# Kernel tuning notes

Measured on AMD Instinct MI355X. Metric: run time of the kernel, lower is better.

## Reference

```python
import jax, jax.numpy as jnp
import numpy as np
from jax import lax

D_MODEL, D_STATE, D_CONV, EXPAND = 512, 16, 4, 2
D_INNER = EXPAND * D_MODEL          # 1024
DT_RANK = (D_MODEL + 15) // 16      # 32
BATCH, SEQ = 4, 1024


def setup_inputs() -> dict:
    key = jax.random.key(0)
    ks = jax.random.split(key, 8)
    s = 0.02
    x = jax.random.normal(ks[0], (BATCH, SEQ, D_MODEL), jnp.float32)
    in_proj_w = jax.random.normal(ks[1], (2 * D_INNER, D_MODEL), jnp.float32) * s
    conv_w = jax.random.normal(ks[2], (D_INNER, 1, D_CONV), jnp.float32) * s  # depthwise
    conv_b = jnp.zeros((D_INNER,), jnp.float32)
    x_proj_w = jax.random.normal(ks[3], (DT_RANK + 2 * D_STATE, D_INNER), jnp.float32) * s
    dt_proj_w = jax.random.normal(ks[4], (D_INNER, DT_RANK), jnp.float32) * s
    dt_proj_b = jax.random.normal(ks[5], (D_INNER,), jnp.float32) * 0.1
    # Mamba S4D-real init: A = -[1..d_state] per channel, stored as log
    A_log = jnp.log(jnp.tile(jnp.arange(1, D_STATE + 1, dtype=jnp.float32)[None, :], (D_INNER, 1)))
    D = jnp.ones((D_INNER,), jnp.float32)
    out_proj_w = jax.random.normal(ks[6], (D_MODEL, D_INNER), jnp.float32) * s
    ln_w = jnp.ones((D_MODEL,), jnp.float32)
    ln_b = jnp.zeros((D_MODEL,), jnp.float32)
    return dict(x=x, in_proj_w=in_proj_w, conv_w=conv_w, conv_b=conv_b,
                x_proj_w=x_proj_w, dt_proj_w=dt_proj_w, dt_proj_b=dt_proj_b,
                A_log=A_log, D=D, out_proj_w=out_proj_w, ln_w=ln_w, ln_b=ln_b)


def _selective_scan(u, delta, A, Bm, Cm, D):
    # u, delta: (B,L,Di); A: (Di,N); Bm, Cm: (B,L,N)
    dA = jnp.exp(delta[..., None] * A)                    # (B,L,Di,N)
    dBu = (delta * u)[..., None] * Bm[:, :, None, :]      # (B,L,Di,N)
    dA_t = jnp.moveaxis(dA, 1, 0)                         # (L,B,Di,N)
    dBu_t = jnp.moveaxis(dBu, 1, 0)
    C_t = jnp.moveaxis(Cm, 1, 0)                          # (L,B,N)

    def step(h, inp):
        dA_i, dBu_i, C_i = inp
        h = dA_i * h + dBu_i                              # (B,Di,N)
        y = jnp.einsum('bdn,bn->bd', h, C_i)
        return h, y

    h0 = jnp.zeros((u.shape[0], A.shape[0], A.shape[1]), u.dtype)
    _, ys = lax.scan(step, h0, (dA_t, dBu_t, C_t))        # ys: (L,B,Di)
    return jnp.moveaxis(ys, 0, 1) + u * D                 # (B,L,Di)


def reference(x, in_proj_w, conv_w, conv_b, x_proj_w, dt_proj_w, dt_proj_b,
              A_log, D, out_proj_w, ln_w, ln_b):
    # ---- Mamba SSM ----
    xz = jnp.einsum('bld,ed->ble', x, in_proj_w)          # (B,L,2*Di)
    xs, z = jnp.split(xz, 2, axis=-1)
    # causal depthwise conv over time
    xt = jnp.moveaxis(xs, 1, 2)                           # (B,Di,L)
    xt = lax.conv_general_dilated(xt, conv_w, window_strides=(1,),
                                  padding=[(D_CONV - 1, 0)],
                                  feature_group_count=D_INNER,
                                  dimension_numbers=('NCH', 'OIH', 'NCH'))
    xt = xt + conv_b[None, :, None]
    u = jax.nn.silu(jnp.moveaxis(xt, 1, 2))               # (B,L,Di)

    x_dbl = jnp.einsum('bld,ed->ble', u, x_proj_w)        # (B,L,dt_rank+2N)
    dt = x_dbl[..., :DT_RANK]
    Bm = x_dbl[..., DT_RANK:DT_RANK + D_STATE]
    Cm = x_dbl[..., DT_RANK + D_STATE:]
    delta = jax.nn.softplus(jnp.einsum('blr,dr->bld', dt, dt_proj_w) + dt_proj_b)
    A = -jnp.exp(A_log)                                   # (Di,N)

    y = _selective_scan(u, delta, A, Bm, Cm, D)
    y = y * jax.nn.silu(z)
    ssm_out = jnp.einsum('ble,de->bld', y, out_proj_w)    # (B,L,Dm)

    # ---- residual + LayerNorm ----
    r = x + ssm_out
    mu = jnp.mean(r, axis=-1, keepdims=True)
    var = jnp.mean(jnp.square(r - mu), axis=-1, keepdims=True)
    return (r - mu) / jnp.sqrt(var + 1e-5) * ln_w + ln_b
```

## Files before the change

### kernel.cpp

```cpp
#include <hip/hip_runtime.h>
#include <hip/hip_bf16.h>
#include <math.h>

#define B_   4
#define L_   1024
#define DM   512
#define DI   1024
#define NS   16
#define XDC  64
#define BL   4096
#define G_   8
#define SEG  128

typedef short bfrag __attribute__((ext_vector_type(8)));
typedef float ffrag __attribute__((ext_vector_type(4)));

__device__ __forceinline__ ushort f2bf(float v) {
    __hip_bfloat16 h = __float2bfloat16(v);
    return *(ushort*)&h;
}

__global__ __launch_bounds__(256) void cast_bf16(const float* __restrict__ in,
        ushort* __restrict__ out, int n4)
{
    int i = blockIdx.x * 256 + threadIdx.x;
    if (i >= n4) return;
    float4 v = ((const float4*)in)[i];
    ushort4 o;
    o.x = f2bf(v.x); o.y = f2bf(v.y); o.z = f2bf(v.z); o.w = f2bf(v.w);
    ((ushort4*)out)[i] = o;
}

template<int EPI>
__global__ __launch_bounds__(256) void gemm_mfma(const ushort* __restrict__ A,
        const ushort* __restrict__ B, float* __restrict__ C,
        int K, int ldc, const float* __restrict__ resid)
{
    __shared__ ushort As[128][40];
    __shared__ ushort Bs[128][40];
    const int tid = threadIdx.x;
    const int lane = tid & 63, wave = tid >> 6;
    const int wm = (wave & 1) * 64, wn = (wave >> 1) * 64;
    const int l15 = lane & 15, quad = lane >> 4;
    const int m0 = blockIdx.y * 128, n0 = blockIdx.x * 128;

    ffrag acc[4][4] = {};

    for (int k0 = 0; k0 < K; k0 += 32) {
        #pragma unroll
        for (int i = 0; i < 2; i++) {
            int chunk = tid + i * 256;
            int row = chunk >> 2, kk8 = (chunk & 3) * 8;
            *(uint4*)&As[row][kk8] = *(const uint4*)&A[(size_t)(m0 + row) * K + k0 + kk8];
            *(uint4*)&Bs[row][kk8] = *(const uint4*)&B[(size_t)(n0 + row) * K + k0 + kk8];
        }
        __syncthreads();
        bfrag af[4], bfv[4];
        #pragma unroll
        for (int i = 0; i < 4; i++) {
            af[i]  = *(const bfrag*)&As[wm + i * 16 + l15][quad * 8];
            bfv[i] = *(const bfrag*)&Bs[wn + i * 16 + l15][quad * 8];
        }
        #pragma unroll
        for (int i = 0; i < 4; i++)
            #pragma unroll
            for (int j = 0; j < 4; j++)
                acc[i][j] = __builtin_amdgcn_mfma_f32_16x16x32_bf16(af[i], bfv[j], acc[i][j], 0, 0, 0);
        __syncthreads();
    }

    #pragma unroll
    for (int i = 0; i < 4; i++) {
        #pragma unroll
        for (int j = 0; j < 4; j++) {
            int n = n0 + wn + j * 16 + l15;
            #pragma unroll
            for (int r = 0; r < 4; r++) {
                int m = m0 + wm + i * 16 + quad * 4 + r;
                float v = acc[i][j][r];
                if (EPI == 2) v += resid[(size_t)m * ldc + n];
                C[(size_t)m * ldc + n] = v;
            }
        }
    }
}

template<int MT>
__global__ __launch_bounds__(256) void gemm_tn(const float* __restrict__ A,
        const float* __restrict__ W, float* __restrict__ C,
        int N, int K, int lda, int ldw, int ldc, int atrans,
        int epi, const float* __restrict__ bias)
{
    __shared__ float As[16][MT + 4];
    __shared__ float Ws[16][68];
    const int tid = threadIdx.x;
    const int tx = tid & 15, ty = tid >> 4;
    const int n0 = blockIdx.x * 64, m0 = blockIdx.y * MT;
    const int RM = MT / 16;
    float acc[RM][4] = {};

    for (int k0 = 0; k0 < K; k0 += 16) {
        const int nchunk = MT * 4;
        if (atrans) {
            #pragma unroll
            for (int i = 0; i < (nchunk + 255) / 256; i++) {
                int idx = tid + i * 256;
                if (nchunk < 256 * (i + 1) && idx >= nchunk) break;
                int k = idx / (MT / 4), m4 = (idx % (MT / 4)) * 4;
                const float4 v = *(const float4*)&A[(size_t)(k0 + k) * lda + m0 + m4];
                As[k][m4 + 0] = v.x; As[k][m4 + 1] = v.y;
                As[k][m4 + 2] = v.z; As[k][m4 + 3] = v.w;
            }
        } else {
            #pragma unroll
            for (int i = 0; i < (nchunk + 255) / 256; i++) {
                int idx = tid + i * 256;
                if (nchunk < 256 * (i + 1) && idx >= nchunk) break;
                int r = idx >> 2, c4 = (idx & 3) * 4;
                const float4 v = *(const float4*)&A[(size_t)(m0 + r) * lda + k0 + c4];
                As[c4 + 0][r] = v.x; As[c4 + 1][r] = v.y;
                As[c4 + 2][r] = v.z; As[c4 + 3][r] = v.w;
            }
        }
        {
            int r = tid >> 2, c4 = (tid & 3) * 4;
            const float4 v = *(const float4*)&W[(size_t)(n0 + r) * ldw + k0 + c4];
            Ws[c4 + 0][r] = v.x; Ws[c4 + 1][r] = v.y;
            Ws[c4 + 2][r] = v.z; Ws[c4 + 3][r] = v.w;
        }
        __syncthreads();
        #pragma unroll
        for (int kk = 0; kk < 16; kk++) {
            float a[RM], b[4];
            #pragma unroll
            for (int i = 0; i < RM; i++) a[i] = As[kk][ty * RM + i];
            #pragma unroll
            for (int j = 0; j < 4; j++) b[j] = Ws[kk][tx * 4 + j];
            #pragma unroll
            for (int i = 0; i < RM; i++)
                #pragma unroll
                for (int j = 0; j < 4; j++)
                    acc[i][j] = fmaf(a[i], b[j], acc[i][j]);
        }
        __syncthreads();
    }

    #pragma unroll
    for (int i = 0; i < RM; i++) {
        int m = m0 + ty * RM + i;
        int nb = n0 + tx * 4;
        float4 v = make_float4(acc[i][0], acc[i][1], acc[i][2], acc[i][3]);
        if (epi == 3) {
            float bm = bias[m];
            v.x += bm; v.y += bm; v.z += bm; v.w += bm;
            v.x = (v.x > 20.f) ? v.x : log1pf(__expf(v.x));
            v.y = (v.y > 20.f) ? v.y : log1pf(__expf(v.y));
            v.z = (v.z > 20.f) ? v.z : log1pf(__expf(v.z));
            v.w = (v.w > 20.f) ? v.w : log1pf(__expf(v.w));
        }
        *(float4*)&C[(size_t)m * ldc + nb] = v;
    }
}

__global__ __launch_bounds__(256) void conv_silu(const float* __restrict__ xzT,
        const float* __restrict__ cw, const float* __restrict__ cb,
        float* __restrict__ uT)
{
    int i = blockIdx.x * 256 + threadIdx.x;
    int d  = i >> 10;
    int q  = i & 1023;
    int bl = q * 4;
    int l  = bl & (L_ - 1);
    const float* row = xzT + (size_t)d * BL;
    float4 cur = *(const float4*)&row[bl];
    float4 prev = make_float4(0.f, 0.f, 0.f, 0.f);
    if (l != 0) prev = *(const float4*)&row[bl - 4];
    float v[7] = { prev.y, prev.z, prev.w, cur.x, cur.y, cur.z, cur.w };
    float w0 = cw[d * 4 + 0], w1 = cw[d * 4 + 1], w2 = cw[d * 4 + 2], w3 = cw[d * 4 + 3];
    float bias = cb[d];
    float4 o;
    o.x = bias + w0 * v[0] + w1 * v[1] + w2 * v[2] + w3 * v[3];
    o.y = bias + w0 * v[1] + w1 * v[2] + w2 * v[3] + w3 * v[4];
    o.z = bias + w0 * v[2] + w1 * v[3] + w2 * v[4] + w3 * v[5];
    o.w = bias + w0 * v[3] + w1 * v[4] + w2 * v[5] + w3 * v[6];
    o.x = o.x / (1.f + __expf(-o.x));
    o.y = o.y / (1.f + __expf(-o.y));
    o.z = o.z / (1.f + __expf(-o.z));
    o.w = o.w / (1.f + __expf(-o.w));
    *(float4*)&uT[(size_t)d * BL + bl] = o;
}

__global__ __launch_bounds__(256) void scan_part1(const float* __restrict__ deltaT,
        const float* __restrict__ uT, const float* __restrict__ xdbl,
        const float* __restrict__ A_log, float* __restrict__ h_end,
        float* __restrict__ Sdv)
{
    const int t = blockIdx.x * 256 + threadIdx.x;
    const int n = t & 15;
    const int seg = (t >> 4) & (G_ - 1);
    const int d = (t >> 7) & (DI - 1);
    const int b = t >> 17;

    const float Acoef = -__expf(A_log[d * NS + n]);
    float h = 0.f, sdv = 0.f;

    const size_t base_t = (size_t)d * BL + b * L_ + seg * SEG;
    const size_t base_x = (size_t)b * L_ * XDC + (size_t)seg * SEG * XDC;

    for (int l0 = 0; l0 < SEG; l0 += 16) {
        float dv[16], uv[16], Bv[16];
        {
            const float4* dp = (const float4*)(deltaT + base_t + l0);
            const float4* up = (const float4*)(uT + base_t + l0);
            #pragma unroll
            for (int i = 0; i < 4; i++) {
                *(float4*)&dv[i * 4] = dp[i];
                *(float4*)&uv[i * 4] = up[i];
            }
        }
        {
            const float* xp = xdbl + base_x + (size_t)l0 * XDC + 32 + n;
            #pragma unroll
            for (int j = 0; j < 16; j++) Bv[j] = xp[j * XDC];
        }
        #pragma unroll
        for (int j = 0; j < 16; j++) {
            sdv += dv[j];
            Bv[j] *= dv[j] * uv[j];
            dv[j] = __expf(dv[j] * Acoef);
        }
        #pragma unroll
        for (int j = 0; j < 16; j++)
            h = fmaf(dv[j], h, Bv[j]);
    }
    const int si = ((b * DI + d) * G_ + seg);
    h_end[si * NS + n] = h;
    if (n == 0) Sdv[si] = sdv;
}

__global__ __launch_bounds__(256) void scan_part2(const float* __restrict__ h_end,
        const float* __restrict__ Sdv, const float* __restrict__ A_log,
        float* __restrict__ h0)
{
    const int t = blockIdx.x * 256 + threadIdx.x;
    const int n = t & 15;
    const int g = t >> 4;
    const int d = g & (DI - 1);
    const float Acoef = -__expf(A_log[d * NS + n]);
    float H = 0.f;
    #pragma unroll
    for (int s = 0; s < G_; s++) {
        const int si = g * G_ + s;
        h0[si * NS + n] = H;
        H = h_end[si * NS + n] + __expf(Acoef * Sdv[si]) * H;
    }
}

__global__ __launch_bounds__(256) void scan_part3(const float* __restrict__ deltaT,
        const float* __restrict__ uT, const float* __restrict__ xdbl,
        const float* __restrict__ xzT, const float* __restrict__ A_log,
        const float* __restrict__ Dp, const float* __restrict__ h0,
        float* __restrict__ yT)
{
    const int t = blockIdx.x * 256 + threadIdx.x;
    const int n = t & 15;
    const int seg = (t >> 4) & (G_ - 1);
    const int d = (t >> 7) & (DI - 1);
    const int b = t >> 17;

    const float Acoef = -__expf(A_log[d * NS + n]);
    const float Dd = Dp[d];
    float h = h0[((b * DI + d) * G_ + seg) * NS + n];

    const size_t base_t = (size_t)d * BL + b * L_ + seg * SEG;
    const size_t base_z = (size_t)(DI + d) * BL + b * L_ + seg * SEG;
    const size_t base_x = (size_t)b * L_ * XDC + (size_t)seg * SEG * XDC;

    for (int l0 = 0; l0 < SEG; l0 += 16) {
        float ug = uT [base_t + l0 + n];
        float zg = xzT[base_z + l0 + n];

        float dv[16], uv[16];
        {
            const float4* dp = (const float4*)(deltaT + base_t + l0);
            const float4* up = (const float4*)(uT + base_t + l0);
            #pragma unroll
            for (int i = 0; i < 4; i++) {
                *(float4*)&dv[i * 4] = dp[i];
                *(float4*)&uv[i * 4] = up[i];
            }
        }
        float Bv[16], Cv[16];
        {
            const float* xp = xdbl + base_x + (size_t)l0 * XDC + 32 + n;
            #pragma unroll
            for (int j = 0; j < 16; j++) {
                Bv[j] = xp[j * XDC];
                Cv[j] = xp[j * XDC + 16];
            }
        }
        #pragma unroll
        for (int j = 0; j < 16; j++) {
            Bv[j] *= dv[j] * uv[j];
            dv[j] = __expf(dv[j] * Acoef);
        }
        float p[16];
        #pragma unroll
        for (int j = 0; j < 16; j++) {
            h = fmaf(dv[j], h, Bv[j]);
            p[j] = h * Cv[j];
        }

        float q8[8];
        #pragma unroll
        for (int k = 0; k < 8; k++) {
            float tt = (n & 8) ? p[k] : p[k + 8];
            float rr = __shfl_xor(tt, 8);
            q8[k] = ((n & 8) ? p[k + 8] : p[k]) + rr;
        }
        float q4[4];
        #pragma unroll
        for (int k = 0; k < 4; k++) {
            float tt = (n & 4) ? q8[k] : q8[k + 4];
            float rr = __shfl_xor(tt, 4);
            q4[k] = ((n & 4) ? q8[k + 4] : q8[k]) + rr;
        }
        float q2[2];
        #pragma unroll
        for (int k = 0; k < 2; k++) {
            float tt = (n & 2) ? q4[k] : q4[k + 2];
            float rr = __shfl_xor(tt, 2);
            q2[k] = ((n & 2) ? q4[k + 2] : q4[k]) + rr;
        }
        float tt = (n & 1) ? q2[0] : q2[1];
        float rr = __shfl_xor(tt, 1);
        float S = ((n & 1) ? q2[1] : q2[0]) + rr;

        float v = S + ug * Dd;
        v *= zg / (1.f + __expf(-zg));
        yT[base_t + l0 + n] = v;
    }
}

__global__ __launch_bounds__(256) void transpose_cast(const float* __restrict__ yT,
        ushort* __restrict__ yB)
{
    __shared__ float t[64][65];
    const int bl0 = blockIdx.x * 64, d0 = blockIdx.y * 64;
    const int tid = threadIdx.x;
    #pragma unroll
    for (int i = 0; i < 4; i++) {
        int chunk = tid + i * 256;
        int dr = chunk >> 4, c4 = (chunk & 15) * 4;
        const float4 v = *(const float4*)&yT[(size_t)(d0 + dr) * BL + bl0 + c4];
        t[dr][c4 + 0] = v.x; t[dr][c4 + 1] = v.y;
        t[dr][c4 + 2] = v.z; t[dr][c4 + 3] = v.w;
    }
    __syncthreads();
    #pragma unroll
    for (int i = 0; i < 4; i++) {
        int chunk = tid + i * 256;
        int br = chunk >> 4, dc4 = (chunk & 15) * 4;
        ushort4 o;
        o.x = f2bf(t[dc4 + 0][br]); o.y = f2bf(t[dc4 + 1][br]);
        o.z = f2bf(t[dc4 + 2][br]); o.w = f2bf(t[dc4 + 3][br]);
        *(ushort4*)&yB[(size_t)(bl0 + br) * DI + d0 + dc4] = o;
    }
}

__global__ __launch_bounds__(256) void ln_kernel(const float* __restrict__ r,
        const float* __restrict__ lnw, const float* __restrict__ lnb,
        float* __restrict__ out)
{
    int row = blockIdx.x;
    const float* rr = r + (size_t)row * DM;
    float v0 = rr[threadIdx.x], v1 = rr[threadIdx.x + 256];
    float s = v0 + v1, s2 = v0 * v0 + v1 * v1;
    #pragma unroll
    for (int off = 32; off > 0; off >>= 1) {
        s  += __shfl_down(s, off);
        s2 += __shfl_down(s2, off);
    }
    __shared__ float ls[4], ls2[4];
    __shared__ float mu_s, rstd_s;
    int wid = threadIdx.x >> 6, lane = threadIdx.x & 63;
    if (lane == 0) { ls[wid] = s; ls2[wid] = s2; }
    __syncthreads();
    if (threadIdx.x == 0) {
        float S = ls[0] + ls[1] + ls[2] + ls[3];
        float S2 = ls2[0] + ls2[1] + ls2[2] + ls2[3];
        float mu = S * (1.f / DM);
        float var = S2 * (1.f / DM) - mu * mu;
        mu_s = mu;
        rstd_s = rsqrtf(var + 1e-5f);
    }
    __syncthreads();
    float mu = mu_s, rstd = rstd_s;
    out[(size_t)row * DM + threadIdx.x] =
        (v0 - mu) * rstd * lnw[threadIdx.x] + lnb[threadIdx.x];
    out[(size_t)row * DM + threadIdx.x + 256] =
        (v1 - mu) * rstd * lnw[threadIdx.x + 256] + lnb[threadIdx.x + 256];
}

extern "C" void kernel_launch(void* const* d_in, const int* in_sizes, int n_in,
                              void* d_out, int out_size, void* d_ws, size_t ws_size,
                              hipStream_t stream)
{
    const float* x         = (const float*)d_in[0];
    const float* in_proj_w = (const float*)d_in[1];
    const float* conv_w    = (const float*)d_in[2];
    const float* conv_b    = (const float*)d_in[3];
    const float* x_proj_w  = (const float*)d_in[4];
    const float* dt_proj_w = (const float*)d_in[5];
    const float* dt_proj_b = (const float*)d_in[6];
    const float* A_log     = (const float*)d_in[7];
    const float* Dvec      = (const float*)d_in[8];
    const float* out_proj_w= (const float*)d_in[9];
    const float* ln_w      = (const float*)d_in[10];
    const float* ln_b      = (const float*)d_in[11];
    float* out = (float*)d_out;

    float* ws     = (float*)d_ws;
    float* xzT    = ws;
    float* uT     = xzT    + (size_t)2048 * BL;
    float* xdbl   = uT     + (size_t)DI * BL;
    float* deltaT = xdbl   + (size_t)BL * XDC;
    float* yT     = deltaT + (size_t)DI * BL;
    float* r      = yT     + (size_t)DI * BL;
    ushort* xB    = (ushort*)yT;
    ushort* yB    = (ushort*)deltaT;
    ushort* wOutB = (ushort*)deltaT + (size_t)4 * 1024 * 1024;
    ushort* wInB  = (ushort*)deltaT + (size_t)9 * 1024 * 1024 / 2;
    float* h_end  = r;
    float* h0     = r + (size_t)B_ * DI * G_ * NS;
    float* Sdv    = h0 + (size_t)B_ * DI * G_ * NS;

    dim3 blk(256);

    cast_bf16<<<(BL * DM / 4 + 255) / 256, blk, 0, stream>>>(x, xB, BL * DM / 4);
    cast_bf16<<<(2048 * DM / 4 + 255) / 256, blk, 0, stream>>>(in_proj_w, wInB, 2048 * DM / 4);

    gemm_mfma<0><<<dim3(BL / 128, 2048 / 128), blk, 0, stream>>>(
        wInB, xB, xzT, DM, BL, nullptr);

    conv_silu<<<(DI * BL / 4) / 256, blk, 0, stream>>>(xzT, conv_w, conv_b, uT);

    gemm_tn<32><<<dim3(1, BL / 32), blk, 0, stream>>>(
        uT, x_proj_w, xdbl, XDC, DI, BL, DI, XDC, 1, 0, nullptr);

    gemm_tn<128><<<dim3(BL / 64, DI / 128), blk, 0, stream>>>(
        dt_proj_w, xdbl, deltaT, BL, 32, 32, XDC, BL, 0, 3, dt_proj_b);

    scan_part1<<<(B_ * DI * G_ * NS) / 256, blk, 0, stream>>>(
        deltaT, uT, xdbl, A_log, h_end, Sdv);
    scan_part2<<<(B_ * DI * NS) / 256, blk, 0, stream>>>(
        h_end, Sdv, A_log, h0);
    scan_part3<<<(B_ * DI * G_ * NS) / 256, blk, 0, stream>>>(
        deltaT, uT, xdbl, xzT, A_log, Dvec, h0, yT);

    transpose_cast<<<dim3(BL / 64, DI / 64), blk, 0, stream>>>(yT, yB);
    cast_bf16<<<(DM * DI / 4 + 255) / 256, blk, 0, stream>>>(out_proj_w, wOutB, DM * DI / 4);

    gemm_mfma<2><<<dim3(DM / 128, BL / 128), blk, 0, stream>>>(
        yB, wOutB, r, DI, DM, x);

    ln_kernel<<<BL, blk, 0, stream>>>(r, ln_w, ln_b, out);
}
```

Before: 303.4 us.

## Split-K the x_proj GEMM and double scan segments for more parallelism

Replaces the x_proj GEMM, which launched only 128 blocks, with a 4-way split-K kernel plus a separate reduction kernel, so roughly four times as many blocks run over the long K=1024 dimension. The chunked selective scan now uses 16 segments of 64 steps instead of 8 of 128. This doubles the thread count in the scan passes and halves the serial length of each segment. The costs are extra partial-sum traffic, one more launch, and a longer serial carry chain in scan_part2; Sdv is moved into the yT workspace region.

New measurement: 271.1 us. -10.6%, faster.

```diff
diff --git a/kernel.cpp b/kernel.cpp
--- a/kernel.cpp
+++ b/kernel.cpp
@@ -9,8 +9,9 @@
 #define NS   16
 #define XDC  64
 #define BL   4096
-#define G_   8
-#define SEG  128
+#define G_   16
+#define SEG  64
+#define KS   4
 
 typedef short bfrag __attribute__((ext_vector_type(8)));
 typedef float ffrag __attribute__((ext_vector_type(4)));
@@ -85,42 +86,26 @@
     }
 }
 
-template<int MT>
-__global__ __launch_bounds__(256) void gemm_tn(const float* __restrict__ A,
+__global__ __launch_bounds__(256) void gemm_tn128(const float* __restrict__ A,
         const float* __restrict__ W, float* __restrict__ C,
-        int N, int K, int lda, int ldw, int ldc, int atrans,
-        int epi, const float* __restrict__ bias)
-{
-    __shared__ float As[16][MT + 4];
+        int N, int K, int lda, int ldw, int ldc,
+        const float* __restrict__ bias)
+{
+    __shared__ float As[16][132];
     __shared__ float Ws[16][68];
     const int tid = threadIdx.x;
     const int tx = tid & 15, ty = tid >> 4;
-    const int n0 = blockIdx.x * 64, m0 = blockIdx.y * MT;
-    const int RM = MT / 16;
-    float acc[RM][4] = {};
+    const int n0 = blockIdx.x * 64, m0 = blockIdx.y * 128;
+    float acc[8][4] = {};
 
     for (int k0 = 0; k0 < K; k0 += 16) {
-        const int nchunk = MT * 4;
-        if (atrans) {
-            #pragma unroll
-            for (int i = 0; i < (nchunk + 255) / 256; i++) {
-                int idx = tid + i * 256;
-                if (nchunk < 256 * (i + 1) && idx >= nchunk) break;
-                int k = idx / (MT / 4), m4 = (idx % (MT / 4)) * 4;
-                const float4 v = *(const float4*)&A[(size_t)(k0 + k) * lda + m0 + m4];
-                As[k][m4 + 0] = v.x; As[k][m4 + 1] = v.y;
-                As[k][m4 + 2] = v.z; As[k][m4 + 3] = v.w;
-            }
-        } else {
-            #pragma unroll
-            for (int i = 0; i < (nchunk + 255) / 256; i++) {
-                int idx = tid + i * 256;
-                if (nchunk < 256 * (i + 1) && idx >= nchunk) break;
-                int r = idx >> 2, c4 = (idx & 3) * 4;
-                const float4 v = *(const float4*)&A[(size_t)(m0 + r) * lda + k0 + c4];
-                As[c4 + 0][r] = v.x; As[c4 + 1][r] = v.y;
-                As[c4 + 2][r] = v.z; As[c4 + 3][r] = v.w;
-            }
+        #pragma unroll
+        for (int i = 0; i < 2; i++) {
+            int idx = tid * 2 + i;
+            int r = idx >> 2, c4 = (idx & 3) * 4;
+            const float4 v = *(const float4*)&A[(size_t)(m0 + r) * lda + k0 + c4];
+            As[c4 + 0][r] = v.x; As[c4 + 1][r] = v.y;
+            As[c4 + 2][r] = v.z; As[c4 + 3][r] = v.w;
         }
         {
             int r = tid >> 2, c4 = (tid & 3) * 4;
@@ -131,13 +116,13 @@
         __syncthreads();
         #pragma unroll
         for (int kk = 0; kk < 16; kk++) {
-            float a[RM], b[4];
-            #pragma unroll
-            for (int i = 0; i < RM; i++) a[i] = As[kk][ty * RM + i];
+            float a[8], b[4];
+            #pragma unroll
+            for (int i = 0; i < 8; i++) a[i] = As[kk][ty * 8 + i];
             #pragma unroll
             for (int j = 0; j < 4; j++) b[j] = Ws[kk][tx * 4 + j];
             #pragma unroll
-            for (int i = 0; i < RM; i++)
+            for (int i = 0; i < 8; i++)
                 #pragma unroll
                 for (int j = 0; j < 4; j++)
                     acc[i][j] = fmaf(a[i], b[j], acc[i][j]);
@@ -146,20 +131,82 @@
     }
 
     #pragma unroll
-    for (int i = 0; i < RM; i++) {
-        int m = m0 + ty * RM + i;
+    for (int i = 0; i < 8; i++) {
+        int m = m0 + ty * 8 + i;
         int nb = n0 + tx * 4;
         float4 v = make_float4(acc[i][0], acc[i][1], acc[i][2], acc[i][3]);
-        if (epi == 3) {
-            float bm = bias[m];
-            v.x += bm; v.y += bm; v.z += bm; v.w += bm;
-            v.x = (v.x > 20.f) ? v.x : log1pf(__expf(v.x));
-            v.y = (v.y > 20.f) ? v.y : log1pf(__expf(v.y));
-            v.z = (v.z > 20.f) ? v.z : log1pf(__expf(v.z));
-            v.w = (v.w > 20.f) ? v.w : log1pf(__expf(v.w));
-        }
+        float bm = bias[m];
+        v.x += bm; v.y += bm; v.z += bm; v.w += bm;
+        v.x = (v.x > 20.f) ? v.x : log1pf(__expf(v.x));
+        v.y = (v.y > 20.f) ? v.y : log1pf(__expf(v.y));
+        v.z = (v.z > 20.f) ? v.z : log1pf(__expf(v.z));
+        v.w = (v.w > 20.f) ? v.w : log1pf(__expf(v.w));
         *(float4*)&C[(size_t)m * ldc + nb] = v;
     }
+}
+
+__global__ __launch_bounds__(256) void gemm3_splitk(const float* __restrict__ uT,
+        const float* __restrict__ xw, float* __restrict__ part)
+{
+    __shared__ float As[16][33];
+    __shared__ float Ws[16][68];
+    const int tid = threadIdx.x;
+    const int tx = tid & 15, ty = tid >> 4;
+    const int ks = blockIdx.x, m0 = blockIdx.y * 32;
+    const int kbase = ks * (DI / KS);
+    float acc[2][4] = {};
+
+    for (int k0 = 0; k0 < DI / KS; k0 += 16) {
+        if (tid < 128) {
+            int k = tid >> 3, m4 = (tid & 7) * 4;
+            const float4 v = *(const float4*)&uT[(size_t)(kbase + k0 + k) * BL + m0 + m4];
+            As[k][m4 + 0] = v.x; As[k][m4 + 1] = v.y;
+            As[k][m4 + 2] = v.z; As[k][m4 + 3] = v.w;
+        }
+        {
+            int r = tid >> 2, c4 = (tid & 3) * 4;
+            const float4 v = *(const float4*)&xw[(size_t)r * DI + kbase + k0 + c4];
+            Ws[c4 + 0][r] = v.x; Ws[c4 + 1][r] = v.y;
+            Ws[c4 + 2][r] = v.z; Ws[c4 + 3][r] = v.w;
+        }
+        __syncthreads();
+        #pragma unroll
+        for (int kk = 0; kk < 16; kk++) {
+            float a[2], b[4];
+            a[0] = As[kk][ty * 2 + 0];
+            a[1] = As[kk][ty * 2 + 1];
+            #pragma unroll
+            for (int j = 0; j < 4; j++) b[j] = Ws[kk][tx * 4 + j];
+            #pragma unroll
+            for (int i = 0; i < 2; i++)
+                #pragma unroll
+                for (int j = 0; j < 4; j++)
+                    acc[i][j] = fmaf(a[i], b[j], acc[i][j]);
+        }
+        __syncthreads();
+    }
+
+    float* pp = part + (size_t)ks * BL * XDC;
+    #pragma unroll
+    for (int i = 0; i < 2; i++) {
+        int m = m0 + ty * 2 + i;
+        *(float4*)&pp[(size_t)m * XDC + tx * 4] =
+            make_float4(acc[i][0], acc[i][1], acc[i][2], acc[i][3]);
+    }
+}
+
+__global__ __launch_bounds__(256) void gemm3_reduce(const float* __restrict__ part,
+        float* __restrict__ xdbl)
+{
+    int i = blockIdx.x * 256 + threadIdx.x;
+    const float4* p0 = (const float4*)part;
+    float4 a = p0[i];
+    #pragma unroll
+    for (int s = 1; s < KS; s++) {
+        float4 b = p0[i + (size_t)s * BL * XDC / 4];
+        a.x += b.x; a.y += b.y; a.z += b.z; a.w += b.w;
+    }
+    ((float4*)xdbl)[i] = a;
 }
 
 __global__ __launch_bounds__(256) void conv_silu(const float* __restrict__ xzT,
@@ -198,8 +245,8 @@
     const int t = blockIdx.x * 256 + threadIdx.x;
     const int n = t & 15;
     const int seg = (t >> 4) & (G_ - 1);
-    const int d = (t >> 7) & (DI - 1);
-    const int b = t >> 17;
+    const int d = (t >> 8) & (DI - 1);
+    const int b = t >> 18;
 
     const float Acoef = -__expf(A_log[d * NS + n]);
     float h = 0.f, sdv = 0.f;
@@ -265,8 +312,8 @@
     const int t = blockIdx.x * 256 + threadIdx.x;
     const int n = t & 15;
     const int seg = (t >> 4) & (G_ - 1);
-    const int d = (t >> 7) & (DI - 1);
-    const int b = t >> 17;
+    const int d = (t >> 8) & (DI - 1);
+    const int b = t >> 18;
 
     const float Acoef = -__expf(A_log[d * NS + n]);
     const float Dd = Dp[d];
@@ -428,12 +475,13 @@
     float* yT     = deltaT + (size_t)DI * BL;
     float* r      = yT     + (size_t)DI * BL;
     ushort* xB    = (ushort*)yT;
+    float*  xdblp = yT;
+    float*  Sdv   = yT + (size_t)KS * BL * XDC;
     ushort* yB    = (ushort*)deltaT;
     ushort* wOutB = (ushort*)deltaT + (size_t)4 * 1024 * 1024;
     ushort* wInB  = (ushort*)deltaT + (size_t)9 * 1024 * 1024 / 2;
     float* h_end  = r;
     float* h0     = r + (size_t)B_ * DI * G_ * NS;
-    float* Sdv    = h0 + (size_t)B_ * DI * G_ * NS;
 
     dim3 blk(256);
 
@@ -445,11 +493,11 @@
 
     conv_silu<<<(DI * BL / 4) / 256, blk, 0, stream>>>(xzT, conv_w, conv_b, uT);
 
-    gemm_tn<32><<<dim3(1, BL / 32), blk, 0, stream>>>(
-        uT, x_proj_w, xdbl, XDC, DI, BL, DI, XDC, 1, 0, nullptr);
-
-    gemm_tn<128><<<dim3(BL / 64, DI / 128), blk, 0, stream>>>(
-        dt_proj_w, xdbl, deltaT, BL, 32, 32, XDC, BL, 0, 3, dt_proj_b);
+    gemm3_splitk<<<dim3(KS, BL / 32), blk, 0, stream>>>(uT, x_proj_w, xdblp);
+    gemm3_reduce<<<(BL * XDC / 4) / 256, blk, 0, stream>>>(xdblp, xdbl);
+
+    gemm_tn128<<<dim3(BL / 64, DI / 128), blk, 0, stream>>>(
+        dt_proj_w, xdbl, deltaT, BL, 32, 32, XDC, BL, dt_proj_b);
 
     scan_part1<<<(B_ * DI * G_ * NS) / 256, blk, 0, stream>>>(
         deltaT, uT, xdbl, A_log, h_end, Sdv);
```
